# Performance work log

Hardware: AMD Instinct MI355X
Metric: run time of the kernel (lower is better)

## Reference

```python
import jax, jax.numpy as jnp
import numpy as np

N_ATOMS = 200000   # total atoms in batch
N_NBR   = 10       # max neighbors per atom (a2a width)
N_MOLS  = 8000     # molecules in batch (25 atoms each)
HID     = 128      # hidden_size
FDIM    = 151      # raw atom feature dim (GROVER default)
FEAT    = 200      # molecule-level descriptor dim
DFF     = 4 * HID  # PositionwiseFeedForward inner dim
FFN_H   = 256      # mol_atom_from_atom_ffn hidden
TASKS   = 12       # num_tasks
EPS     = 1e-6     # GROVER LayerNorm eps


def setup_inputs() -> dict:
    key = jax.random.key(0)
    ks = jax.random.split(key, 14)
    s = 0.02
    atoms_per_mol = N_ATOMS // N_MOLS
    starts = (jnp.arange(N_MOLS, dtype=jnp.int32) * atoms_per_mol)
    sizes = jnp.full((N_MOLS,), atoms_per_mol, dtype=jnp.int32)
    a_scope = jnp.stack([starts, sizes], axis=1)  # [M, 2]
    return {
        "atom_output": jax.random.normal(ks[0], (N_ATOMS, HID), jnp.float32),
        "original_f_atoms": jax.random.normal(ks[1], (N_ATOMS, FDIM), jnp.float32),
        "features_batch": jax.random.normal(ks[2], (N_MOLS, FEAT), jnp.float32),
        "a2a": jax.random.randint(ks[3], (N_ATOMS, N_NBR), 0, N_ATOMS, jnp.int32),
        "a_scope": a_scope,
        # PositionwiseFeedForward (ffn_atom_from_atom): in = FDIM + HID
        "W1": jax.random.normal(ks[4], (FDIM + HID, DFF), jnp.float32) * s,
        "b1": jnp.zeros((DFF,), jnp.float32),
        "W2": jax.random.normal(ks[5], (DFF, HID), jnp.float32) * s,
        "b2": jnp.zeros((HID,), jnp.float32),
        # SublayerConnection LayerNorm
        "gamma": jnp.ones((HID,), jnp.float32),
        "beta": jnp.zeros((HID,), jnp.float32),
        # mol_atom_from_atom_ffn: in = HID + FEAT
        "Wf1": jax.random.normal(ks[6], (HID + FEAT, FFN_H), jnp.float32) * s,
        "bf1": jnp.zeros((FFN_H,), jnp.float32),
        "Wf2": jax.random.normal(ks[7], (FFN_H, TASKS), jnp.float32) * s,
        "bf2": jnp.zeros((TASKS,), jnp.float32),
    }


def _layernorm(x, gamma, beta):
    mu = jnp.mean(x, axis=-1, keepdims=True)
    var = jnp.mean((x - mu) ** 2, axis=-1, keepdims=True)
    return gamma * (x - mu) * jax.lax.rsqrt(var + EPS) + beta


def reference(atom_output, original_f_atoms, features_batch, a2a, a_scope,
              W1, b1, W2, b2, gamma, beta, Wf1, bf1, Wf2, bf2):
    # select_neighbor_and_aggregate: gather neighbor embeddings, sum over nbrs
    aggr = jnp.sum(atom_output[a2a], axis=1)                      # [N, HID]
    x = jnp.concatenate([original_f_atoms, aggr], axis=1)         # [N, FDIM+HID]
    # PositionwiseFeedForward (eval: dropout = identity)
    h = jax.nn.relu(x @ W1 + b1)
    ffn_out = h @ W2 + b2                                         # [N, HID]
    # SublayerConnection(None, x) -> dropout(LayerNorm(x))
    atom_emb = _layernorm(ffn_out, gamma, beta)                   # [N, HID]
    # Readout: mean-pool per molecule via a_scope (start, size)
    starts = a_scope[:, 0]
    sizes = a_scope[:, 1].astype(atom_emb.dtype)
    seg = jnp.searchsorted(starts, jnp.arange(atom_emb.shape[0], dtype=starts.dtype), side="right") - 1
    mol = jax.ops.segment_sum(atom_emb, seg, num_segments=a_scope.shape[0]) / sizes[:, None]
    # concat molecule descriptors, then mol_atom_from_atom_ffn
    mol = jnp.concatenate([mol, features_batch], axis=1)          # [M, HID+FEAT]
    out = jax.nn.relu(mol @ Wf1 + bf1) @ Wf2 + bf2                # [M, TASKS]
    return out
```

## Files before the change

kernel.cpp:

```cpp
#include <hip/hip_runtime.h>
#include <hip/hip_bf16.h>

#define N_ATOMS 200000
#define N_NBR 10
#define N_MOLS 8000
#define HID 128
#define FDIM 151
#define FEAT 200
#define DFF 512
#define FFN_H 256
#define TASKS 12
#define KX 279
#define K1P 288
#define XSB 288
#define HSB 128
#define FS 132
#define KM 328
#define K3 352
#define MS 360
#define MT 64
#define SMEM_ATOMS (MT * XSB * 2 + MT * HSB * 2)

typedef __hip_bfloat16 bf16;
typedef __attribute__((ext_vector_type(8))) __bf16 bf16x8;
typedef __attribute__((ext_vector_type(4))) float f32x4;

__device__ __forceinline__ float bf2f(bf16 x) { return __bfloat162float(x); }
__device__ __forceinline__ float blo(unsigned w) { union { unsigned u; float f; } c; c.u = w << 16; return c.f; }
__device__ __forceinline__ float bhi(unsigned w) { union { unsigned u; float f; } c; c.u = w & 0xFFFF0000u; return c.f; }

__device__ __forceinline__ int xswz(int r, int e) {
  return r * XSB + (e ^ ((e < 256 ? (r & 7) : (r & 3)) << 3));
}
__device__ __forceinline__ int hswz(int r, int e) {
  return r * HSB + (e ^ ((r & 7) << 3));
}

__global__ void prep_weights_kernel(const float* __restrict__ W1,
                                    const float* __restrict__ W2,
                                    const float* __restrict__ Wf1,
                                    bf16* __restrict__ W1bT,
                                    bf16* __restrict__ W2bT,
                                    bf16* __restrict__ Wf1bT) {
  int idx = blockIdx.x * 256 + threadIdx.x;
  if (idx < DFF * K1P) {
    int n = idx / K1P, k = idx - n * K1P;
    float v;
    if (k < HID)      v = W1[(size_t)(FDIM + k) * DFF + n];
    else if (k < KX)  v = W1[(size_t)(k - HID) * DFF + n];
    else              v = 0.f;
    W1bT[idx] = __float2bfloat16(v);
    return;
  }
  idx -= DFF * K1P;
  if (idx < HID * DFF) {
    int n = idx / DFF, k = idx - n * DFF;
    W2bT[idx] = __float2bfloat16(W2[(size_t)k * HID + n]);
    return;
  }
  idx -= HID * DFF;
  if (idx < FFN_H * K3) {
    int n = idx / K3, k = idx - n * K3;
    float v = (k < KM) ? Wf1[(size_t)k * FFN_H + n] : 0.f;
    Wf1bT[idx] = __float2bfloat16(v);
  }
}

__global__ void conv_ao_kernel(const float* __restrict__ ao, bf16* __restrict__ ao16) {
  const int idx = blockIdx.x * 256 + threadIdx.x;
  const float4 v0 = *(const float4*)&ao[(size_t)idx * 8];
  const float4 v1 = *(const float4*)&ao[(size_t)idx * 8 + 4];
  union { bf16 h[8]; uint4 u; } pk;
  pk.h[0] = __float2bfloat16(v0.x); pk.h[1] = __float2bfloat16(v0.y);
  pk.h[2] = __float2bfloat16(v0.z); pk.h[3] = __float2bfloat16(v0.w);
  pk.h[4] = __float2bfloat16(v1.x); pk.h[5] = __float2bfloat16(v1.y);
  pk.h[6] = __float2bfloat16(v1.z); pk.h[7] = __float2bfloat16(v1.w);
  *(uint4*)&ao16[(size_t)idx * 8] = pk.u;
}

__global__ __launch_bounds__(256)
void gather_kernel(const bf16* __restrict__ ao16,
                   const int* __restrict__ a2a,
                   bf16* __restrict__ aggr) {
  const int gid = blockIdx.x * 256 + threadIdx.x;
  const int atom = gid >> 4, c8 = gid & 15;
  int idxs[N_NBR];
#pragma unroll
  for (int j = 0; j < N_NBR; ++j) idxs[j] = a2a[atom * N_NBR + j];
  float s[8];
#pragma unroll
  for (int e = 0; e < 8; ++e) s[e] = 0.f;
#pragma unroll
  for (int j = 0; j < N_NBR; ++j) {
    const uint4 u = *(const uint4*)&ao16[(size_t)idxs[j] * HID + c8 * 8];
    s[0] += blo(u.x); s[1] += bhi(u.x);
    s[2] += blo(u.y); s[3] += bhi(u.y);
    s[4] += blo(u.z); s[5] += bhi(u.z);
    s[6] += blo(u.w); s[7] += bhi(u.w);
  }
  union { bf16 h[8]; uint4 u; } pk;
#pragma unroll
  for (int e = 0; e < 8; ++e) pk.h[e] = __float2bfloat16(s[e]);
  *(uint4*)&aggr[(size_t)atom * HID + c8 * 8] = pk.u;
}

__global__ __launch_bounds__(512, 6)
void atoms_kernel(const bf16* __restrict__ aggr,
                  const float* __restrict__ f_atoms,
                  const bf16* __restrict__ W1bT,
                  const float* __restrict__ b1,
                  const bf16* __restrict__ W2bT,
                  const float* __restrict__ b2,
                  const float* __restrict__ gamma,
                  const float* __restrict__ beta,
                  bf16* __restrict__ atom_emb) {
  __shared__ char smem[SMEM_ATOMS];
  bf16* Xs = (bf16*)smem;
  bf16* Hs = (bf16*)(smem + MT * XSB * 2);
  float* Fs = (float*)smem;

  const int tid = threadIdx.x;
  const int m0 = blockIdx.x * MT;
  const int lane = tid & 63;
  const int w = tid >> 6;
  const int lr = lane & 15;
  const int lk = lane >> 4;

  {
    int q = tid;
#pragma unroll
    for (int p = 0; p < 2; ++p) {
      const int r = q >> 4, c8 = q & 15;
      *(uint4*)&Xs[r * XSB + ((c8 * 8) ^ ((r & 7) << 3))] =
          *(const uint4*)&aggr[(size_t)(m0 + r) * HID + c8 * 8];
      q += 512;
    }
  }
  {
    const float* fb = &f_atoms[(size_t)m0 * FDIM];
    int q = tid;
#pragma unroll
    for (int p = 0; p < 5; ++p) {
      if (p < 4 || q < (MT * FDIM) / 4) {
        const float4 v = *(const float4*)&fb[q * 4];
        const float vf[4] = { v.x, v.y, v.z, v.w };
        const int flat = q * 4;
        const int r0 = flat / FDIM, c0 = flat - r0 * FDIM;
#pragma unroll
        for (int e = 0; e < 4; ++e) {
          const int cc = c0 + e;
          const int rr = (cc < FDIM) ? r0 : r0 + 1;
          const int ee = HID + ((cc < FDIM) ? cc : cc - FDIM);
          Xs[xswz(rr, ee)] = __float2bfloat16(vf[e]);
        }
      }
      q += 512;
    }
  }
  if (tid < MT * (K1P - KX)) {
    const int r = tid / (K1P - KX), cc = tid - r * (K1P - KX);
    Xs[xswz(r, KX + cc)] = __float2bfloat16(0.f);
  }
  __syncthreads();

  f32x4 acc2[4];
#pragma unroll
  for (int mi = 0; mi < 4; ++mi) acc2[mi] = (f32x4)0.f;

#pragma unroll 1
  for (int pp = 0; pp < 2; ++pp) {
    const int c0 = pp * 2;
    f32x4 acc1[2][4];
#pragma unroll
    for (int c = 0; c < 2; ++c)
#pragma unroll
      for (int mi = 0; mi < 4; ++mi) acc1[c][mi] = (f32x4)0.f;
    {
      const bf16* w1p = &W1bT[(size_t)(c0 * 128 + w * 16 + lr) * K1P + lk * 8];
      __builtin_amdgcn_s_setprio(1);
#pragma unroll
      for (int kk = 0; kk < K1P / 32; ++kk) {
        bf16x8 b0 = *(const bf16x8*)&w1p[kk * 32];
        bf16x8 b1f = *(const bf16x8*)&w1p[(size_t)128 * K1P + kk * 32];
#pragma unroll
        for (int mi = 0; mi < 4; ++mi) {
          const bf16x8 a = *(const bf16x8*)&Xs[xswz(mi * 16 + lr, kk * 32 + lk * 8)];
          acc1[0][mi] = __builtin_amdgcn_mfma_f32_16x16x32_bf16(b0, a, acc1[0][mi], 0, 0, 0);
          acc1[1][mi] = __builtin_amdgcn_mfma_f32_16x16x32_bf16(b1f, a, acc1[1][mi], 0, 0, 0);
        }
      }
      __builtin_amdgcn_s_setprio(0);
    }
#pragma unroll
    for (int c = 0; c < 2; ++c) {
      const int nc = c0 + c;
      {
        const float4 bb = *(const float4*)&b1[nc * 128 + w * 16 + lk * 4];
        const float bbf[4] = { bb.x, bb.y, bb.z, bb.w };
#pragma unroll
        for (int mi = 0; mi < 4; ++mi) {
          union { bf16 h[4]; uint2 u2; } pk;
#pragma unroll
          for (int r = 0; r < 4; ++r) {
            const float h = acc1[c][mi][r] + bbf[r];
            pk.h[r] = __float2bfloat16(h > 0.f ? h : 0.f);
          }
          *(uint2*)&Hs[hswz(mi * 16 + lr, w * 16 + lk * 4)] = pk.u2;
        }
      }
      __syncthreads();
      {
        const bf16* w2p = &W2bT[(size_t)(w * 16 + lr) * DFF + nc * 128 + lk * 8];
        __builtin_amdgcn_s_setprio(1);
#pragma unroll
        for (int kk = 0; kk < 4; ++kk) {
          const bf16x8 wb = *(const bf16x8*)&w2p[kk * 32];
#pragma unroll
          for (int mi = 0; mi < 4; ++mi) {
            const bf16x8 hb = *(const bf16x8*)&Hs[hswz(mi * 16 + lr, kk * 32 + lk * 8)];
            acc2[mi] = __builtin_amdgcn_mfma_f32_16x16x32_bf16(wb, hb, acc2[mi], 0, 0, 0);
          }
        }
        __builtin_amdgcn_s_setprio(0);
      }
      __syncthreads();
    }
  }

  {
    const float4 b2v = *(const float4*)&b2[w * 16 + lk * 4];
#pragma unroll
    for (int mi = 0; mi < 4; ++mi) {
      float4 v;
      v.x = acc2[mi][0] + b2v.x;
      v.y = acc2[mi][1] + b2v.y;
      v.z = acc2[mi][2] + b2v.z;
      v.w = acc2[mi][3] + b2v.w;
      *(float4*)&Fs[(mi * 16 + lr) * FS + w * 16 + lk * 4] = v;
    }
  }
  __syncthreads();

  const float gam0 = gamma[lane], gam1 = gamma[64 + lane];
  const float bet0 = beta[lane],  bet1 = beta[64 + lane];
#pragma unroll
  for (int i = 0; i < MT / 8; ++i) {
    const int row = w * (MT / 8) + i;
    const float x0 = Fs[row * FS + lane];
    const float x1 = Fs[row * FS + 64 + lane];
    float s = x0 + x1;
    float q = x0 * x0 + x1 * x1;
#pragma unroll
    for (int off = 32; off > 0; off >>= 1) {
      s += __shfl_xor(s, off);
      q += __shfl_xor(q, off);
    }
    const float mu = s * (1.f / 128.f);
    const float var = q * (1.f / 128.f) - mu * mu;
    const float rs = rsqrtf(var + 1e-6f);
    const int atom = m0 + row;
    atom_emb[(size_t)atom * HID + lane] =
        __float2bfloat16(gam0 * ((x0 - mu) * rs) + bet0);
    atom_emb[(size_t)atom * HID + 64 + lane] =
        __float2bfloat16(gam1 * ((x1 - mu) * rs) + bet1);
  }
}

__global__ __launch_bounds__(256)
void mol_kernel(const bf16* __restrict__ atom_emb,
                const float* __restrict__ features,
                const int* __restrict__ a_scope,
                bf16* __restrict__ mol_cat) {
  const int tid = threadIdx.x;
  const int mi = tid >> 4, c8 = tid & 15;
  const int base = blockIdx.x * 16;
  const int m = base + mi;
  const int start = a_scope[2 * m];
  const int size  = a_scope[2 * m + 1];
  float s[8];
#pragma unroll
  for (int e = 0; e < 8; ++e) s[e] = 0.f;
  for (int a = 0; a < size; ++a) {
    const uint4 u = *(const uint4*)&atom_emb[(size_t)(start + a) * HID + c8 * 8];
    s[0] += blo(u.x); s[1] += bhi(u.x);
    s[2] += blo(u.y); s[3] += bhi(u.y);
    s[4] += blo(u.z); s[5] += bhi(u.z);
    s[6] += blo(u.w); s[7] += bhi(u.w);
  }
  const float inv = 1.f / (float)size;
  union { bf16 h[8]; uint4 u; } pk;
#pragma unroll
  for (int e = 0; e < 8; ++e) pk.h[e] = __float2bfloat16(s[e] * inv);
  *(uint4*)&mol_cat[(size_t)m * K3 + c8 * 8] = pk.u;
  for (int q = tid; q < 16 * 50; q += 256) {
    const int mm = q / 50, qq = q - mm * 50;
    const float4 v = *(const float4*)&features[(size_t)(base + mm) * FEAT + qq * 4];
    union { bf16 h[4]; uint2 u2; } pf;
    pf.h[0] = __float2bfloat16(v.x); pf.h[1] = __float2bfloat16(v.y);
    pf.h[2] = __float2bfloat16(v.z); pf.h[3] = __float2bfloat16(v.w);
    *(uint2*)&mol_cat[(size_t)(base + mm) * K3 + HID + qq * 4] = pf.u2;
  }
  for (int q = tid; q < 16 * (K3 - KM); q += 256) {
    const int mm = q / (K3 - KM), qq = q - mm * (K3 - KM);
    mol_cat[(size_t)(base + mm) * K3 + KM + qq] = __float2bfloat16(0.f);
  }
}

__global__ __launch_bounds__(512)
void molffn1_kernel(const bf16* __restrict__ mol_cat,
                    const bf16* __restrict__ Wf1bT,
                    const float* __restrict__ bf1,
                    bf16* __restrict__ Hf) {
  __shared__ bf16 As[64 * MS];
  const int tid = threadIdx.x;
  const int m0 = blockIdx.x * 64;
  for (int idx = tid; idx < 64 * (K3 / 8); idx += 512) {
    int rr = idx / (K3 / 8), qv = idx - rr * (K3 / 8);
    *(uint4*)&As[rr * MS + qv * 8] = *(const uint4*)&mol_cat[(size_t)(m0 + rr) * K3 + qv * 8];
  }
  __syncthreads();
  const int lane = tid & 63, w = tid >> 6;
  const int lr = lane & 15, lk = lane >> 4;
  const int wn = w * 32;
  f32x4 acc[4][2];
#pragma unroll
  for (int mi = 0; mi < 4; ++mi)
#pragma unroll
    for (int ni = 0; ni < 2; ++ni) acc[mi][ni] = (f32x4)0.f;
#pragma unroll 3
  for (int kk = 0; kk < K3 / 32; ++kk) {
    bf16x8 a[4], b[2];
#pragma unroll
    for (int mi = 0; mi < 4; ++mi)
      a[mi] = *(const bf16x8*)&As[(mi * 16 + lr) * MS + kk * 32 + lk * 8];
#pragma unroll
    for (int ni = 0; ni < 2; ++ni)
      b[ni] = *(const bf16x8*)&Wf1bT[(size_t)(wn + ni * 16 + lr) * K3 + kk * 32 + lk * 8];
#pragma unroll
    for (int mi = 0; mi < 4; ++mi)
#pragma unroll
      for (int ni = 0; ni < 2; ++ni)
        acc[mi][ni] = __builtin_amdgcn_mfma_f32_16x16x32_bf16(a[mi], b[ni], acc[mi][ni], 0, 0, 0);
  }
#pragma unroll
  for (int ni = 0; ni < 2; ++ni) {
    const int n = wn + ni * 16 + lr;
    const float bias = bf1[n];
#pragma unroll
    for (int mi = 0; mi < 4; ++mi)
#pragma unroll
      for (int rr = 0; rr < 4; ++rr) {
        const int row = mi * 16 + lk * 4 + rr;
        const float h = acc[mi][ni][rr] + bias;
        Hf[(size_t)(m0 + row) * FFN_H + n] = __float2bfloat16(h > 0.f ? h : 0.f);
      }
  }
}

__global__ __launch_bounds__(192)
void molffn2_kernel(const bf16* __restrict__ Hf,
                    const float* __restrict__ Wf2,
                    const float* __restrict__ bias2,
                    float* __restrict__ out) {
  __shared__ float Ws[FFN_H * TASKS];
  const int tid = threadIdx.x;
  for (int i = tid; i < FFN_H * TASKS; i += 192) Ws[i] = Wf2[i];
  __syncthreads();
  const int m = blockIdx.x * 16 + tid / TASKS;
  const int t = tid % TASKS;
  float s = bias2[t];
  for (int k8 = 0; k8 < FFN_H / 8; ++k8) {
    const uint4 u = *(const uint4*)&Hf[(size_t)m * FFN_H + k8 * 8];
    const float h[8] = { blo(u.x), bhi(u.x), blo(u.y), bhi(u.y),
                         blo(u.z), bhi(u.z), blo(u.w), bhi(u.w) };
#pragma unroll
    for (int e = 0; e < 8; ++e) s += h[e] * Ws[(k8 * 8 + e) * TASKS + t];
  }
  out[(size_t)m * TASKS + t] = s;
}

extern "C" void kernel_launch(void* const* d_in, const int* in_sizes, int n_in,
                              void* d_out, int out_size, void* d_ws, size_t ws_size,
                              hipStream_t stream) {
  const float* atom_output = (const float*)d_in[0];
  const float* f_atoms     = (const float*)d_in[1];
  const float* features    = (const float*)d_in[2];
  const int*   a2a         = (const int*)d_in[3];
  const int*   a_scope     = (const int*)d_in[4];
  const float* W1   = (const float*)d_in[5];
  const float* b1   = (const float*)d_in[6];
  const float* W2   = (const float*)d_in[7];
  const float* b2   = (const float*)d_in[8];
  const float* gamma = (const float*)d_in[9];
  const float* beta  = (const float*)d_in[10];
  const float* Wf1  = (const float*)d_in[11];
  const float* bf1  = (const float*)d_in[12];
  const float* Wf2  = (const float*)d_in[13];
  const float* bf2v = (const float*)d_in[14];
  float* out = (float*)d_out;

  char* ws = (char*)d_ws;
  size_t off = 0;
  bf16* W1bT  = (bf16*)(ws + off); off += (size_t)DFF * K1P * 2;
  bf16* W2bT  = (bf16*)(ws + off); off += (size_t)HID * DFF * 2;
  bf16* Wf1bT = (bf16*)(ws + off); off += (size_t)FFN_H * K3 * 2;
  bf16* atom_emb = (bf16*)(ws + off); off += (size_t)N_ATOMS * HID * 2;
  bf16* mol_cat  = (bf16*)(ws + off); off += (size_t)N_MOLS * K3 * 2;
  bf16* Hf       = (bf16*)(ws + off); off += (size_t)N_MOLS * FFN_H * 2;
  bf16* ao16     = (bf16*)(ws + off); off += (size_t)N_ATOMS * HID * 2;
  bf16* aggr = atom_emb;

  hipLaunchKernelGGL(prep_weights_kernel, dim3(1184), dim3(256), 0, stream,
                     W1, W2, Wf1, W1bT, W2bT, Wf1bT);
  hipLaunchKernelGGL(conv_ao_kernel, dim3(N_ATOMS * HID / 8 / 256), dim3(256), 0, stream,
                     atom_output, ao16);
  hipLaunchKernelGGL(gather_kernel, dim3(N_ATOMS * 16 / 256), dim3(256), 0, stream,
                     ao16, a2a, aggr);
  hipLaunchKernelGGL(atoms_kernel, dim3(N_ATOMS / MT), dim3(512), 0, stream,
                     aggr, f_atoms,
                     W1bT, b1, W2bT, b2, gamma, beta, atom_emb);
  hipLaunchKernelGGL(mol_kernel, dim3(N_MOLS / 16), dim3(256), 0, stream,
                     atom_emb, features, a_scope, mol_cat);
  hipLaunchKernelGGL(molffn1_kernel, dim3(N_MOLS / 64), dim3(512), 0, stream,
                     mol_cat, Wf1bT, bf1, Hf);
  hipLaunchKernelGGL(molffn2_kernel, dim3(N_MOLS / 16), dim3(192), 0, stream,
                     Hf, Wf2, bf2v, out);
}
```

Measured before the change: 318.5 us.

## Switch atoms kernel to 32x32x16 MFMA with full-width accumulators and padded LDS

Replaces the 16x16x32 MFMA tiling in the atom FFN kernel with 32x32x16 MFMAs. All four 128-column chunks of the first GEMM are now accumulated in one pass, and the second GEMM is split across waves by row half and column quarter. LDS rows are padded instead of XOR-swizzled, and the f_atoms staging loads and converts 8 elements per thread with vector stores. This cuts LDS reads per flop and instruction count, at the cost of more accumulator registers, with occupancy lowered from 6 to 4 blocks per CU.

```diff
diff --git a/kernel.cpp b/kernel.cpp
--- a/kernel.cpp
+++ b/kernel.cpp
@@ -12,28 +12,25 @@
 #define TASKS 12
 #define KX 279
 #define K1P 288
-#define XSB 288
-#define HSB 128
+#define XSB 296
+#define HSB 136
 #define FS 132
 #define KM 328
 #define K3 352
 #define MS 360
 #define MT 64
-#define SMEM_ATOMS (MT * XSB * 2 + MT * HSB * 2)
 
 typedef __hip_bfloat16 bf16;
 typedef __attribute__((ext_vector_type(8))) __bf16 bf16x8;
 typedef __attribute__((ext_vector_type(4))) float f32x4;
+typedef __attribute__((ext_vector_type(16))) float f32x16;
 
 __device__ __forceinline__ float bf2f(bf16 x) { return __bfloat162float(x); }
 __device__ __forceinline__ float blo(unsigned w) { union { unsigned u; float f; } c; c.u = w << 16; return c.f; }
 __device__ __forceinline__ float bhi(unsigned w) { union { unsigned u; float f; } c; c.u = w & 0xFFFF0000u; return c.f; }
 
-__device__ __forceinline__ int xswz(int r, int e) {
-  return r * XSB + (e ^ ((e < 256 ? (r & 7) : (r & 3)) << 3));
-}
 __device__ __forceinline__ int hswz(int r, int e) {
-  return r * HSB + (e ^ ((r & 7) << 3));
+  return r * HSB + (e ^ (((r >> 3) & 3) << 3));
 }
 
 __global__ void prep_weights_kernel(const float* __restrict__ W1,
@@ -104,7 +101,7 @@
   *(uint4*)&aggr[(size_t)atom * HID + c8 * 8] = pk.u;
 }
 
-__global__ __launch_bounds__(512, 6)
+__global__ __launch_bounds__(512, 4)
 void atoms_kernel(const bf16* __restrict__ aggr,
                   const float* __restrict__ f_atoms,
                   const bf16* __restrict__ W1bT,
@@ -114,130 +111,130 @@
                   const float* __restrict__ gamma,
                   const float* __restrict__ beta,
                   bf16* __restrict__ atom_emb) {
-  __shared__ char smem[SMEM_ATOMS];
-  bf16* Xs = (bf16*)smem;
-  bf16* Hs = (bf16*)(smem + MT * XSB * 2);
-  float* Fs = (float*)smem;
+  __shared__ bf16 Xs[MT * XSB];
+  __shared__ bf16 Hs[MT * HSB];
+  float* Fs = (float*)Xs;
 
   const int tid = threadIdx.x;
   const int m0 = blockIdx.x * MT;
   const int lane = tid & 63;
   const int w = tid >> 6;
-  const int lr = lane & 15;
-  const int lk = lane >> 4;
+  const int l31 = lane & 31;
+  const int lh = lane >> 5;
 
   {
     int q = tid;
 #pragma unroll
     for (int p = 0; p < 2; ++p) {
       const int r = q >> 4, c8 = q & 15;
-      *(uint4*)&Xs[r * XSB + ((c8 * 8) ^ ((r & 7) << 3))] =
-          *(const uint4*)&aggr[(size_t)(m0 + r) * HID + c8 * 8];
+      *(uint4*)&Xs[r * XSB + c8 * 8] = *(const uint4*)&aggr[(size_t)(m0 + r) * HID + c8 * 8];
       q += 512;
     }
   }
   {
     const float* fb = &f_atoms[(size_t)m0 * FDIM];
-    int q = tid;
-#pragma unroll
-    for (int p = 0; p < 5; ++p) {
-      if (p < 4 || q < (MT * FDIM) / 4) {
-        const float4 v = *(const float4*)&fb[q * 4];
-        const float vf[4] = { v.x, v.y, v.z, v.w };
-        const int flat = q * 4;
-        const int r0 = flat / FDIM, c0 = flat - r0 * FDIM;
-#pragma unroll
-        for (int e = 0; e < 4; ++e) {
-          const int cc = c0 + e;
-          const int rr = (cc < FDIM) ? r0 : r0 + 1;
-          const int ee = HID + ((cc < FDIM) ? cc : cc - FDIM);
-          Xs[xswz(rr, ee)] = __float2bfloat16(vf[e]);
+    int u = tid;
+#pragma unroll
+    for (int p = 0; p < 3; ++p) {
+      if (p < 2 || u < MT * 19) {
+        const int row = u / 19, o = u - row * 19;
+        const float* src = &fb[row * FDIM + o * 8];
+        float vf[8];
+        if (o < 18) {
+          const float4 va = *(const float4*)src;
+          const float4 vb = *(const float4*)(src + 4);
+          vf[0] = va.x; vf[1] = va.y; vf[2] = va.z; vf[3] = va.w;
+          vf[4] = vb.x; vf[5] = vb.y; vf[6] = vb.z; vf[7] = vb.w;
+        } else {
+          const float4 va = *(const float4*)src;
+          vf[0] = va.x; vf[1] = va.y; vf[2] = va.z; vf[3] = va.w;
+          vf[4] = src[4]; vf[5] = src[5]; vf[6] = src[6]; vf[7] = 0.f;
+        }
+        union { bf16 h[8]; uint4 q4; } pk;
+#pragma unroll
+        for (int e = 0; e < 8; ++e) pk.h[e] = __float2bfloat16(vf[e]);
+        *(uint4*)&Xs[row * XSB + HID + o * 8] = pk.q4;
+      }
+      u += 512;
+    }
+  }
+  if (tid < MT) {
+    const uint4 z = {0u, 0u, 0u, 0u};
+    *(uint4*)&Xs[tid * XSB + 280] = z;
+  }
+  __syncthreads();
+
+  f32x16 acc1[2][2];
+#pragma unroll
+  for (int t = 0; t < 2; ++t)
+#pragma unroll
+    for (int mt = 0; mt < 2; ++mt) acc1[t][mt] = (f32x16)0.f;
+  {
+    const bf16* w1p0 = &W1bT[(size_t)(w * 32 + l31) * K1P + lh * 8];
+    const bf16* w1p1 = w1p0 + (size_t)256 * K1P;
+    __builtin_amdgcn_s_setprio(1);
+#pragma unroll 6
+    for (int kk = 0; kk < 18; ++kk) {
+      const bf16x8 b0 = *(const bf16x8*)&w1p0[kk * 16];
+      const bf16x8 b1f = *(const bf16x8*)&w1p1[kk * 16];
+      const bf16x8 a0 = *(const bf16x8*)&Xs[l31 * XSB + kk * 16 + lh * 8];
+      const bf16x8 a1 = *(const bf16x8*)&Xs[(32 + l31) * XSB + kk * 16 + lh * 8];
+      acc1[0][0] = __builtin_amdgcn_mfma_f32_32x32x16_bf16(b0, a0, acc1[0][0], 0, 0, 0);
+      acc1[0][1] = __builtin_amdgcn_mfma_f32_32x32x16_bf16(b0, a1, acc1[0][1], 0, 0, 0);
+      acc1[1][0] = __builtin_amdgcn_mfma_f32_32x32x16_bf16(b1f, a0, acc1[1][0], 0, 0, 0);
+      acc1[1][1] = __builtin_amdgcn_mfma_f32_32x32x16_bf16(b1f, a1, acc1[1][1], 0, 0, 0);
+    }
+    __builtin_amdgcn_s_setprio(0);
+  }
+
+  const int wm = w & 1, wq = w >> 1;
+  f32x16 acc2 = (f32x16)0.f;
+#pragma unroll
+  for (int nc = 0; nc < 4; ++nc) {
+    if ((w >> 2) == (nc & 1)) {
+      const int t = nc >> 1;
+#pragma unroll
+      for (int g = 0; g < 4; ++g) {
+        const int nl = (w & 3) * 32 + 8 * g + 4 * lh;
+        const float4 bb = *(const float4*)&b1[nc * 128 + nl];
+        const float bbf[4] = { bb.x, bb.y, bb.z, bb.w };
+#pragma unroll
+        for (int mt = 0; mt < 2; ++mt) {
+          union { bf16 h[4]; uint2 u2; } pk;
+#pragma unroll
+          for (int r4 = 0; r4 < 4; ++r4) {
+            const float h = acc1[t][mt][g * 4 + r4] + bbf[r4];
+            pk.h[r4] = __float2bfloat16(h > 0.f ? h : 0.f);
+          }
+          *(uint2*)&Hs[hswz(mt * 32 + l31, nl)] = pk.u2;
         }
       }
-      q += 512;
-    }
-  }
-  if (tid < MT * (K1P - KX)) {
-    const int r = tid / (K1P - KX), cc = tid - r * (K1P - KX);
-    Xs[xswz(r, KX + cc)] = __float2bfloat16(0.f);
-  }
-  __syncthreads();
-
-  f32x4 acc2[4];
-#pragma unroll
-  for (int mi = 0; mi < 4; ++mi) acc2[mi] = (f32x4)0.f;
-
-#pragma unroll 1
-  for (int pp = 0; pp < 2; ++pp) {
-    const int c0 = pp * 2;
-    f32x4 acc1[2][4];
-#pragma unroll
-    for (int c = 0; c < 2; ++c)
-#pragma unroll
-      for (int mi = 0; mi < 4; ++mi) acc1[c][mi] = (f32x4)0.f;
+    }
+    __syncthreads();
     {
-      const bf16* w1p = &W1bT[(size_t)(c0 * 128 + w * 16 + lr) * K1P + lk * 8];
+      const bf16* w2p = &W2bT[(size_t)(wq * 32 + l31) * DFF + nc * 128 + lh * 8];
       __builtin_amdgcn_s_setprio(1);
 #pragma unroll
-      for (int kk = 0; kk < K1P / 32; ++kk) {
-        bf16x8 b0 = *(const bf16x8*)&w1p[kk * 32];
-        bf16x8 b1f = *(const bf16x8*)&w1p[(size_t)128 * K1P + kk * 32];
-#pragma unroll
-        for (int mi = 0; mi < 4; ++mi) {
-          const bf16x8 a = *(const bf16x8*)&Xs[xswz(mi * 16 + lr, kk * 32 + lk * 8)];
-          acc1[0][mi] = __builtin_amdgcn_mfma_f32_16x16x32_bf16(b0, a, acc1[0][mi], 0, 0, 0);
-          acc1[1][mi] = __builtin_amdgcn_mfma_f32_16x16x32_bf16(b1f, a, acc1[1][mi], 0, 0, 0);
-        }
+      for (int kk = 0; kk < 8; ++kk) {
+        const bf16x8 wb = *(const bf16x8*)&w2p[kk * 16];
+        const bf16x8 hb = *(const bf16x8*)&Hs[hswz(wm * 32 + l31, kk * 16 + lh * 8)];
+        acc2 = __builtin_amdgcn_mfma_f32_32x32x16_bf16(wb, hb, acc2, 0, 0, 0);
       }
       __builtin_amdgcn_s_setprio(0);
     }
-#pragma unroll
-    for (int c = 0; c < 2; ++c) {
-      const int nc = c0 + c;
-      {
-        const float4 bb = *(const float4*)&b1[nc * 128 + w * 16 + lk * 4];
-        const float bbf[4] = { bb.x, bb.y, bb.z, bb.w };
-#pragma unroll
-        for (int mi = 0; mi < 4; ++mi) {
-          union { bf16 h[4]; uint2 u2; } pk;
-#pragma unroll
-          for (int r = 0; r < 4; ++r) {
-            const float h = acc1[c][mi][r] + bbf[r];
-            pk.h[r] = __float2bfloat16(h > 0.f ? h : 0.f);
-          }
-          *(uint2*)&Hs[hswz(mi * 16 + lr, w * 16 + lk * 4)] = pk.u2;
-        }
-      }
-      __syncthreads();
-      {
-        const bf16* w2p = &W2bT[(size_t)(w * 16 + lr) * DFF + nc * 128 + lk * 8];
-        __builtin_amdgcn_s_setprio(1);
-#pragma unroll
-        for (int kk = 0; kk < 4; ++kk) {
-          const bf16x8 wb = *(const bf16x8*)&w2p[kk * 32];
-#pragma unroll
-          for (int mi = 0; mi < 4; ++mi) {
-            const bf16x8 hb = *(const bf16x8*)&Hs[hswz(mi * 16 + lr, kk * 32 + lk * 8)];
-            acc2[mi] = __builtin_amdgcn_mfma_f32_16x16x32_bf16(wb, hb, acc2[mi], 0, 0, 0);
-          }
-        }
-        __builtin_amdgcn_s_setprio(0);
-      }
-      __syncthreads();
-    }
-  }
-
-  {
-    const float4 b2v = *(const float4*)&b2[w * 16 + lk * 4];
-#pragma unroll
-    for (int mi = 0; mi < 4; ++mi) {
-      float4 v;
-      v.x = acc2[mi][0] + b2v.x;
-      v.y = acc2[mi][1] + b2v.y;
-      v.z = acc2[mi][2] + b2v.z;
-      v.w = acc2[mi][3] + b2v.w;
-      *(float4*)&Fs[(mi * 16 + lr) * FS + w * 16 + lk * 4] = v;
-    }
+    __syncthreads();
+  }
+
+#pragma unroll
+  for (int g = 0; g < 4; ++g) {
+    const int n2 = wq * 32 + 8 * g + 4 * lh;
+    const float4 bb = *(const float4*)&b2[n2];
+    float4 v;
+    v.x = acc2[g * 4 + 0] + bb.x;
+    v.y = acc2[g * 4 + 1] + bb.y;
+    v.z = acc2[g * 4 + 2] + bb.z;
+    v.w = acc2[g * 4 + 3] + bb.w;
+    *(float4*)&Fs[(wm * 32 + l31) * FS + n2] = v;
   }
   __syncthreads();
 
```

After: 355.2 us. +11.5%, slower.
